# Kernel optimization log

Hardware: AMD Instinct MI355X
Metric: run time of the kernel (lower is better)

Reference implementation:

```python
import jax, jax.numpy as jnp
import numpy as np

N, TI, TO1 = 8, 200, 51
V, E, H, J, L = 1024, 512, 512, 512, 3
ENC_D = 512


def setup_inputs() -> dict:
    key = jax.random.key(0)
    ks = jax.random.split(key, 11)
    s = lambda k, shape, sc: jax.random.normal(k, shape, jnp.float32) * sc
    return {
        "enc_out": s(ks[0], (N, TI, ENC_D), 1.0),
        "tgt_pad": jax.random.randint(ks[1], (N, TO1), 0, V),
        "embed": s(ks[2], (V, E), 0.02),          # nn.Embedding weight
        "w_ih": s(ks[3], (L, 4 * H, E), 0.04),    # LSTM input-hidden (gate order i,f,g,o)
        "w_hh": s(ks[4], (L, 4 * H, H), 0.04),    # LSTM hidden-hidden
        "b_ih": s(ks[5], (L, 4 * H), 0.04),
        "b_hh": s(ks[6], (L, 4 * H), 0.04),
        "enc_w": s(ks[7], (J, ENC_D), 0.04),      # enc_proj (no bias)
        "dec_w": s(ks[8], (J, H), 0.04),          # dec_proj weight
        "dec_b": s(ks[9], (J,), 0.04),            # dec_proj bias
        "out_w": s(ks[10], (V, J), 0.04),         # output (no bias)
    }


def lstm_layer(x, wih, whh, bih, bhh):
    # x: [N, T, E] -> [N, T, H]; PyTorch LSTM gate order i, f, g, o
    n = x.shape[0]
    h0 = jnp.zeros((n, whh.shape[1]), x.dtype)
    c0 = jnp.zeros_like(h0)
    gin = jnp.einsum('nte,ge->ntg', x, wih) + bih + bhh  # precompute input contributions

    def step(carry, g_t):
        h, c = carry
        g = g_t + h @ whh.T
        i, f, gg, o = jnp.split(g, 4, axis=-1)
        c = jax.nn.sigmoid(f) * c + jax.nn.sigmoid(i) * jnp.tanh(gg)
        h = jax.nn.sigmoid(o) * jnp.tanh(c)
        return (h, c), h

    _, hs = jax.lax.scan(step, (h0, c0), jnp.swapaxes(gin, 0, 1))
    return jnp.swapaxes(hs, 0, 1)


def reference(enc_out, tgt_pad, embed, w_ih, w_hh, b_ih, b_hh, enc_w, dec_w, dec_b, out_w):
    # embedding lookup
    x = embed[tgt_pad]                                   # [N, To+1, E]
    # 3-layer unidirectional LSTM
    for l in range(w_ih.shape[0]):
        x = lstm_layer(x, w_ih[l], w_hh[l], b_ih[l], b_hh[l])
    # projections
    enc_p = jnp.einsum('ntd,jd->ntj', enc_out, enc_w)    # [N, Ti, J]
    dec_p = jnp.einsum('nud,jd->nuj', x, dec_w) + dec_b  # [N, To+1, J]
    # joint: broadcast add -> tanh -> output linear (no bias)
    add = enc_p[:, :, None, :] + dec_p[:, None, :, :]    # [N, Ti, To+1, J]
    return jnp.einsum('ntuj,vj->ntuv', jnp.tanh(add), out_w)  # [N, Ti, To+1, V]
```

## Files before the change

kernel.cpp:

```cpp
#include <hip/hip_runtime.h>
#include <cstdint>
#include <cstddef>

typedef __attribute__((ext_vector_type(4))) float f32x4;
typedef __attribute__((ext_vector_type(8))) short bf16x8;
typedef __attribute__((ext_vector_type(8))) unsigned short u16x8;
typedef __attribute__((ext_vector_type(4))) float float4v;
typedef __attribute__((ext_vector_type(2))) unsigned long long u64x2;
typedef unsigned long long ull;

#define NB   8
#define TIN  200
#define TO1  51
#define VSZ  1024
#define HSZ  512
static constexpr int MJOINT = NB * TIN * TO1;
static constexpr int MROWS  = TO1 * NB;

static constexpr size_t B_ENCBF = 0;
static constexpr size_t B_ENCW  = B_ENCBF + 1664ull*512*2;
static constexpr size_t B_DECW  = B_ENCW  + 512ull*512*2;
static constexpr size_t B_OUTW  = B_DECW  + 512ull*512*2;
static constexpr size_t B_WIH   = B_OUTW  + 1024ull*512*2;
static constexpr size_t B_WHH   = B_WIH   + 3ull*2048*512*2;
static constexpr size_t B_XTR   = B_WHH   + 3ull*2048*512*2;
static constexpr size_t B_BSUM  = B_XTR   + 4ull*408*512*2;
static constexpr size_t B_FLAGS = B_BSUM  + 3ull*2048*4;
static constexpr size_t B_ENCP  = B_FLAGS + 8192;
static constexpr size_t B_DECP  = B_ENCP  + 1664ull*512*4;
static constexpr size_t B_ABUF  = B_DECP  + 512ull*512*4;

__device__ __forceinline__ unsigned short f2bf(float f) {
  union { float f; unsigned u; } v; v.f = f;
  unsigned r = v.u + 0x7FFFu + ((v.u >> 16) & 1u);
  return (unsigned short)(r >> 16);
}
__device__ __forceinline__ float fast_tanh(float x) {
  float t = __expf(2.0f * x);
  return 1.0f - 2.0f / (t + 1.0f);
}
__device__ __forceinline__ float fast_sig(float x) {
  return 1.0f / (1.0f + __expf(-x));
}
__device__ __forceinline__ void gll16(const void* g, void* l) {
  __builtin_amdgcn_global_load_lds(
      (const __attribute__((address_space(1))) unsigned int*)g,
      (__attribute__((address_space(3))) unsigned int*)l, 16, 0, 0);
}
__device__ __forceinline__ void cvt8(const float* s, unsigned short* d) {
  const float4v* sp = (const float4v*)s;
  float4v x = sp[0], y = sp[1];
  u16x8 o;
  o[0]=f2bf(x[0]); o[1]=f2bf(x[1]); o[2]=f2bf(x[2]); o[3]=f2bf(x[3]);
  o[4]=f2bf(y[0]); o[5]=f2bf(y[1]); o[6]=f2bf(y[2]); o[7]=f2bf(y[3]);
  *(u16x8*)d = o;
}

static constexpr int N_ENC  = 102400;
static constexpr int N_ENCW = 32768;
static constexpr int N_DECW = 32768;
static constexpr int N_OUTW = 65536;
static constexpr int N_WIH  = 393216;
static constexpr int P0 = N_ENC, P1 = P0+N_ENCW, P2 = P1+N_DECW, P3 = P2+N_OUTW,
                     P4 = P3+N_WIH;

__global__ __launch_bounds__(256) void cvt_all(const float* __restrict__ enc,
                                               const float* __restrict__ encw,
                                               const float* __restrict__ decw,
                                               const float* __restrict__ outw,
                                               const float* __restrict__ wih,
                                               const float* __restrict__ whh,
                                               unsigned short* __restrict__ d_enc,
                                               unsigned short* __restrict__ d_encw,
                                               unsigned short* __restrict__ d_decw,
                                               unsigned short* __restrict__ d_outw,
                                               unsigned short* __restrict__ d_wih,
                                               unsigned short* __restrict__ d_whh,
                                               int* __restrict__ flags) {
  if (blockIdx.x == 0 && threadIdx.x < 96) flags[threadIdx.x * 16] = 0;
  int i = blockIdx.x * 256 + threadIdx.x;
  const float* s; unsigned short* d; int rel;
  if      (i < P0) { s = enc;  d = d_enc;  rel = i; }
  else if (i < P1) { s = encw; d = d_encw; rel = i - P0; }
  else if (i < P2) { s = decw; d = d_decw; rel = i - P1; }
  else if (i < P3) { s = outw; d = d_outw; rel = i - P2; }
  else if (i < P4) { s = wih;  d = d_wih;  rel = i - P3; }
  else             { s = whh;  d = d_whh;  rel = i - P4; }
  cvt8(s + (size_t)rel * 8, d + (size_t)rel * 8);
}

__global__ __launch_bounds__(256) void bsum_kernel(const float* __restrict__ a,
                                                   const float* __restrict__ b,
                                                   float* __restrict__ o, int n) {
  int i = blockIdx.x * 256 + threadIdx.x;
  if (i < n) o[i] = a[i] + b[i];
}

__global__ __launch_bounds__(256) void embed_kernel(const float* __restrict__ emb,
                                                    const int* __restrict__ tgt,
                                                    unsigned short* __restrict__ x0) {
  int idx = blockIdx.x * 256 + threadIdx.x;
  if (idx >= MROWS * 64) return;
  int m = idx >> 6, kc = (idx & 63) * 8;
  int t = m >> 3, n = m & 7;
  int v = tgt[n * TO1 + t];
  cvt8(emb + (size_t)v * 512 + kc, x0 + (size_t)m * 512 + kc);
}

__global__ __launch_bounds__(256) void gemm_bf16(const unsigned short* __restrict__ A,
                                                 const unsigned short* __restrict__ B,
                                                 float* __restrict__ C,
                                                 const float* __restrict__ bias,
                                                 int M, int N, int K) {
  __shared__ __align__(16) unsigned short lds[2][2][4096];
  const int tid = threadIdx.x;
  const int wave = tid >> 6, lane = tid & 63;
  const int lr = lane & 15, lg = lane >> 4;
  const int wm = (wave >> 1) * 64, wn = (wave & 1) * 64;
  const int xsl = (lg ^ (lr & 3)) << 3;

  const int nwg = gridDim.x * gridDim.y;
  const int id = blockIdx.y * gridDim.x + blockIdx.x;
  const int q = nwg >> 3, r = nwg & 7, xcd = id & 7, rest = id >> 3;
  const int nid = (xcd < r ? xcd * (q + 1) : r * (q + 1) + (xcd - r) * q) + rest;
  const size_t n0 = (size_t)(nid % gridDim.x) * 128;
  const size_t m0 = (size_t)(nid / gridDim.x) * 128;

  f32x4 acc[4][4];
#pragma unroll
  for (int i = 0; i < 4; ++i)
#pragma unroll
    for (int j = 0; j < 4; ++j) acc[i][j] = (f32x4){0.f, 0.f, 0.f, 0.f};

#define STAGE(bf, kt)                                                                 \
  do {                                                                                \
    _Pragma("unroll") for (int u = 0; u < 2; ++u) {                                   \
      const int s = u * 256 + tid;                                                    \
      const int row_ = s >> 2;                                                        \
      const int ch = (s & 3) ^ (row_ & 3);                                            \
      gll16(A + (m0 + row_) * (size_t)K + (kt) + ch * 8,                              \
            &lds[bf][0][(u * 256 + wave * 64) * 8]);                                  \
    }                                                                                 \
    _Pragma("unroll") for (int u = 0; u < 2; ++u) {                                   \
      const int s = u * 256 + tid;                                                    \
      const int row_ = s >> 2;                                                        \
      const int ch = (s & 3) ^ (row_ & 3);                                            \
      gll16(B + (n0 + row_) * (size_t)K + (kt) + ch * 8,                              \
            &lds[bf][1][(u * 256 + wave * 64) * 8]);                                  \
    }                                                                                 \
  } while (0)

  const int nt = K >> 5;
  int cur = 0;
  STAGE(0, 0);
  for (int t = 0; t < nt; ++t) {
    if (t + 1 < nt) {
      STAGE(cur ^ 1, (t + 1) * 32);
      asm volatile("s_waitcnt vmcnt(4)" ::: "memory");
    } else {
      asm volatile("s_waitcnt vmcnt(0)" ::: "memory");
    }
    __builtin_amdgcn_s_barrier();
    const unsigned short* As_ = lds[cur][0];
    const unsigned short* Bs_ = lds[cur][1];
    bf16x8 a[4], b[4];
#pragma unroll
    for (int i = 0; i < 4; ++i) a[i] = *(const bf16x8*)&As_[(wm + i * 16 + lr) * 32 + xsl];
#pragma unroll
    for (int j = 0; j < 4; ++j) b[j] = *(const bf16x8*)&Bs_[(wn + j * 16 + lr) * 32 + xsl];
    __builtin_amdgcn_s_setprio(1);
#pragma unroll
    for (int i = 0; i < 4; ++i)
#pragma unroll
      for (int j = 0; j < 4; ++j)
        acc[i][j] = __builtin_amdgcn_mfma_f32_16x16x32_bf16(a[i], b[j], acc[i][j], 0, 0, 0);
    __builtin_amdgcn_s_setprio(0);
    __builtin_amdgcn_s_barrier();
    cur ^= 1;
  }
#undef STAGE

  const int rq = lg * 4;
#pragma unroll
  for (int j = 0; j < 4; ++j) {
    const int col = (int)n0 + wn + j * 16 + lr;
    const float bv = bias ? bias[col] : 0.0f;
#pragma unroll
    for (int i = 0; i < 4; ++i) {
#pragma unroll
      for (int q2 = 0; q2 < 4; ++q2) {
        const long m = (long)m0 + wm + i * 16 + rq + q2;
        if (m < M) C[(size_t)m * N + col] = acc[i][j][q2] + bv;
      }
    }
  }
}

__global__ __launch_bounds__(512, 2) void gemm256(const unsigned short* __restrict__ A,
                                                  const unsigned short* __restrict__ B,
                                                  float* __restrict__ C,
                                                  int M, int N, int K) {
  __shared__ __align__(16) unsigned short lds[2][2][16384];
  const int tid = threadIdx.x;
  const int wave = tid >> 6, lane = tid & 63;
  const int lr = lane & 15, lg = lane >> 4;
  const int wr = (wave >> 2) * 128;
  const int wc = (wave & 3) * 64;

  const int nwg = gridDim.x * gridDim.y;
  const int id = blockIdx.y * gridDim.x + blockIdx.x;
  const int q = nwg >> 3, r = nwg & 7, xcd = id & 7, rest = id >> 3;
  const int nid = (xcd < r ? xcd * (q + 1) : r * (q + 1) + (xcd - r) * q) + rest;
  const size_t n0 = (size_t)(nid % gridDim.x) * 256;
  const size_t m0 = (size_t)(nid / gridDim.x) * 256;

  f32x4 acc[8][4];
#pragma unroll
  for (int i = 0; i < 8; ++i)
#pragma unroll
    for (int j = 0; j < 4; ++j) acc[i][j] = (f32x4){0.f, 0.f, 0.f, 0.f};

#define STG(bf, kt)                                                                    \
  do {                                                                                 \
    _Pragma("unroll") for (int u = 0; u < 4; ++u) {                                    \
      const int idx = u * 512 + tid;                                                   \
      const int row_ = idx >> 3;                                                       \
      const int ch = (idx & 7) ^ (row_ & 7);                                           \
      gll16(A + (m0 + row_) * (size_t)K + (kt) + ch * 8,                               \
            &lds[bf][0][(u * 512 + wave * 64) * 8]);                                   \
    }                                                                                  \
    _Pragma("unroll") for (int u = 0; u < 4; ++u) {                                    \
      const int idx = u * 512 + tid;                                                   \
      const int row_ = idx >> 3;                                                       \
      const int ch = (idx & 7) ^ (row_ & 7);                                           \
      gll16(B + (n0 + row_) * (size_t)K + (kt) + ch * 8,                               \
            &lds[bf][1][(u * 512 + wave * 64) * 8]);                                   \
    }                                                                                  \
  } while (0)

  const int nt = K >> 6;
  int cur = 0;
  STG(0, 0);
  for (int t = 0; t < nt; ++t) {
    if (t + 1 < nt) {
      STG(cur ^ 1, (t + 1) * 64);
      asm volatile("s_waitcnt vmcnt(8)" ::: "memory");
    } else {
      asm volatile("s_waitcnt vmcnt(0)" ::: "memory");
    }
    __builtin_amdgcn_s_barrier();
    const unsigned short* As_ = lds[cur][0];
    const unsigned short* Bs_ = lds[cur][1];
    bf16x8 b[4][2];
#pragma unroll
    for (int p = 0; p < 4; ++p) {
      if (p == 0) {
#pragma unroll
        for (int j = 0; j < 4; ++j) {
          const int rb = wc + j * 16 + lr;
          const int sw = rb & 7;
          b[j][0] = *(const bf16x8*)&Bs_[rb * 64 + ((lg ^ sw) << 3)];
          b[j][1] = *(const bf16x8*)&Bs_[rb * 64 + (((4 + lg) ^ sw) << 3)];
        }
      }
      bf16x8 a[2][2];
#pragma unroll
      for (int i2 = 0; i2 < 2; ++i2) {
        const int ra = wr + (p * 2 + i2) * 16 + lr;
        const int swa = ra & 7;
        a[i2][0] = *(const bf16x8*)&As_[ra * 64 + ((lg ^ swa) << 3)];
        a[i2][1] = *(const bf16x8*)&As_[ra * 64 + (((4 + lg) ^ swa) << 3)];
      }
      __builtin_amdgcn_s_setprio(1);
#pragma unroll
      for (int i2 = 0; i2 < 2; ++i2) {
        const int i = p * 2 + i2;
#pragma unroll
        for (int j = 0; j < 4; ++j) {
          acc[i][j] = __builtin_amdgcn_mfma_f32_16x16x32_bf16(a[i2][0], b[j][0], acc[i][j], 0, 0, 0);
          acc[i][j] = __builtin_amdgcn_mfma_f32_16x16x32_bf16(a[i2][1], b[j][1], acc[i][j], 0, 0, 0);
        }
      }
      __builtin_amdgcn_s_setprio(0);
      __builtin_amdgcn_s_barrier();
    }
    cur ^= 1;
  }
#undef STG

#pragma unroll
  for (int i = 0; i < 8; ++i) {
#pragma unroll
    for (int q2 = 0; q2 < 4; ++q2) {
      const long m = (long)m0 + wr + i * 16 + lg * 4 + q2;
      if (m < M) {
        float* crow = C + (size_t)m * N + n0 + wc;
#pragma unroll
        for (int j = 0; j < 4; ++j) crow[j * 16 + lr] = acc[i][j][q2];
      }
    }
  }
}

__global__ __launch_bounds__(256) void tanha_kernel(const float* __restrict__ encp,
                                                    const float* __restrict__ decp,
                                                    unsigned short* __restrict__ Ab) {
  size_t idx = (size_t)blockIdx.x * 256 + threadIdx.x;
  int m = (int)(idx >> 6);
  int kc = ((int)idx & 63) * 8;
  if (m >= 81664) return;
  u16x8 o;
  if (m >= MJOINT) {
    o[0]=0;o[1]=0;o[2]=0;o[3]=0;o[4]=0;o[5]=0;o[6]=0;o[7]=0;
  } else {
    int n = m / (TIN * TO1);
    int rem = m - n * (TIN * TO1);
    int t = rem / TO1;
    int u = rem - t * TO1;
    const float4v* ep = (const float4v*)(encp + ((size_t)n * TIN + t) * 512 + kc);
    const float4v* dp = (const float4v*)(decp + ((size_t)u * 8 + n) * 512 + kc);
    float4v e0 = ep[0], e1 = ep[1], d0 = dp[0], d1 = dp[1];
    o[0]=f2bf(fast_tanh(e0[0]+d0[0])); o[1]=f2bf(fast_tanh(e0[1]+d0[1]));
    o[2]=f2bf(fast_tanh(e0[2]+d0[2])); o[3]=f2bf(fast_tanh(e0[3]+d0[3]));
    o[4]=f2bf(fast_tanh(e1[0]+d1[0])); o[5]=f2bf(fast_tanh(e1[1]+d1[1]));
    o[6]=f2bf(fast_tanh(e1[2]+d1[2])); o[7]=f2bf(fast_tanh(e1[3]+d1[3]));
  }
  *(u16x8*)(Ab + (size_t)m * 512 + kc) = o;
}

__global__ __launch_bounds__(256) void rnn_enc_kernel(const unsigned short* __restrict__ wih,
                                                      const unsigned short* __restrict__ whh,
                                                      const float* __restrict__ bsum,
                                                      unsigned short* __restrict__ xtr,
                                                      int* __restrict__ flags,
                                                      const unsigned short* __restrict__ eA,
                                                      const unsigned short* __restrict__ eB,
                                                      float* __restrict__ eC) {
  __shared__ __align__(16) unsigned short w_s[64 * 1024];
  __shared__ __align__(16) unsigned short x_s[8 * 512];
  __shared__ __align__(16) unsigned short h_s[8 * 512];
  __shared__ float gates_s[4][8][16];

  const int tid = threadIdx.x;
  const int wave = tid >> 6, lane = tid & 63;
  const int lr = lane & 15, lg = lane >> 4;

  if (blockIdx.x >= 96) {
    unsigned short* eld = w_s;
    const int g = blockIdx.x - 96;
    const int wm = (wave >> 1) * 64, wn = (wave & 1) * 64;
    const int xsl = (lg ^ (lr & 3)) << 3;
    const int nwg = 52;
    const int q = nwg >> 3, r = nwg & 7, xcd = g & 7, rest = g >> 3;
    const int nid = (xcd < r ? xcd * (q + 1) : r * (q + 1) + (xcd - r) * q) + rest;
    const size_t n0 = (size_t)(nid & 3) * 128;
    const size_t m0 = (size_t)(nid >> 2) * 128;

    f32x4 acc[4][4];
#pragma unroll
    for (int i = 0; i < 4; ++i)
#pragma unroll
      for (int j = 0; j < 4; ++j) acc[i][j] = (f32x4){0.f, 0.f, 0.f, 0.f};

#define ESTG(bf, kt)                                                                   \
    do {                                                                               \
      _Pragma("unroll") for (int u = 0; u < 2; ++u) {                                  \
        const int s = u * 256 + tid;                                                   \
        const int row_ = s >> 2;                                                       \
        const int ch = (s & 3) ^ (row_ & 3);                                           \
        gll16(eA + (m0 + row_) * 512 + (kt) + ch * 8,                                  \
              &eld[(bf) * 8192 + (u * 256 + wave * 64) * 8]);                          \
      }                                                                                \
      _Pragma("unroll") for (int u = 0; u < 2; ++u) {                                  \
        const int s = u * 256 + tid;                                                   \
        const int row_ = s >> 2;                                                       \
        const int ch = (s & 3) ^ (row_ & 3);                                           \
        gll16(eB + (n0 + row_) * 512 + (kt) + ch * 8,                                  \
              &eld[(bf) * 8192 + 4096 + (u * 256 + wave * 64) * 8]);                   \
      }                                                                                \
    } while (0)

    int cur = 0;
    ESTG(0, 0);
    for (int t = 0; t < 16; ++t) {
      if (t + 1 < 16) {
        ESTG(cur ^ 1, (t + 1) * 32);
        asm volatile("s_waitcnt vmcnt(4)" ::: "memory");
      } else {
        asm volatile("s_waitcnt vmcnt(0)" ::: "memory");
      }
      __builtin_amdgcn_s_barrier();
      const unsigned short* As_ = eld + cur * 8192;
      const unsigned short* Bs_ = As_ + 4096;
      bf16x8 a[4], b[4];
#pragma unroll
      for (int i = 0; i < 4; ++i) a[i] = *(const bf16x8*)&As_[(wm + i * 16 + lr) * 32 + xsl];
#pragma unroll
      for (int j = 0; j < 4; ++j) b[j] = *(const bf16x8*)&Bs_[(wn + j * 16 + lr) * 32 + xsl];
      __builtin_amdgcn_s_setprio(1);
#pragma unroll
      for (int i = 0; i < 4; ++i)
#pragma unroll
        for (int j = 0; j < 4; ++j)
          acc[i][j] = __builtin_amdgcn_mfma_f32_16x16x32_bf16(a[i], b[j], acc[i][j], 0, 0, 0);
      __builtin_amdgcn_s_setprio(0);
      __builtin_amdgcn_s_barrier();
      cur ^= 1;
    }
#undef ESTG

    const int rq = lg * 4;
#pragma unroll
    for (int j = 0; j < 4; ++j) {
      const int col = (int)n0 + wn + j * 16 + lr;
#pragma unroll
      for (int i = 0; i < 4; ++i) {
#pragma unroll
        for (int q2 = 0; q2 < 4; ++q2) {
          const long m = (long)m0 + wm + i * 16 + rq + q2;
          eC[(size_t)m * 512 + col] = acc[i][j][q2];
        }
      }
    }
    return;
  }

  const int l = blockIdx.x >> 5;
  const int b32 = blockIdx.x & 31;
  const int hid0 = b32 << 4;
  const int r7 = lr & 7;
  const int rw = wave * 16 + lr;

  {
    const int rl = tid >> 2;
    const int qt = tid & 3;
    const size_t R = (size_t)l * 2048 + (size_t)(rl >> 4) * 512 + hid0 + (rl & 15);
    const unsigned short* s0 = wih + R * 512;
    const unsigned short* s1 = whh + R * 512;
#pragma unroll
    for (int i = 0; i < 32; ++i) {
      int c = qt * 32 + i;
      bf16x8 wv = (c < 64) ? *(const bf16x8*)&s0[c * 8] : *(const bf16x8*)&s1[(c - 64) * 8];
      *(bf16x8*)&w_s[rl * 1024 + ((c ^ (rl & 7)) << 3)] = wv;
    }
  }
  const float bias = bsum[(size_t)l * 2048 + (size_t)wave * 512 + hid0 + lr];

  const unsigned short* xin = xtr + (size_t)l * MROWS * 512;
  unsigned short* xout = xtr + (size_t)(l + 1) * MROWS * 512;
  float c_reg = 0.f;
  const int srow = tid >> 5;
  const int sc = tid & 31;
  __syncthreads();

#define ALOAD(P) __hip_atomic_load((P), __ATOMIC_RELAXED, __HIP_MEMORY_SCOPE_AGENT)

  f32x4 ax0, ax1;

  if (l > 0) {
    if (wave == 0) {
      for (;;) {
        bool ok_ = true;
        if (lane < 32)
          ok_ = ALOAD(&flags[((l - 1) * 32 + lane) * 16]) >= 1;
        if (__all(ok_)) break;
        __builtin_amdgcn_s_sleep(1);
      }
    }
  }
  __syncthreads();
  {
    const ull* px = (const ull*)(xin + (size_t)srow * 512);
#pragma unroll
    for (int k_ = 0; k_ < 2; ++k_) {
      const int c_ = sc + k_ * 32;
      ull v0 = ALOAD(px + c_ * 2), v1 = ALOAD(px + c_ * 2 + 1);
      *(u64x2*)&x_s[srow * 512 + ((c_ ^ srow) << 3)] = (u64x2){v0, v1};
    }
  }
  __syncthreads();
  ax0 = (f32x4){0.f, 0.f, 0.f, 0.f};
  ax1 = (f32x4){0.f, 0.f, 0.f, 0.f};
#pragma unroll
  for (int c16 = 0; c16 < 16; ++c16) {
    const int cc = c16 * 4 + lg;
    bf16x8 av = *(const bf16x8*)&x_s[r7 * 512 + ((cc ^ r7) << 3)];
    bf16x8 bv = *(const bf16x8*)&w_s[rw * 1024 + ((cc ^ r7) << 3)];
    if (c16 & 1) ax1 = __builtin_amdgcn_mfma_f32_16x16x32_bf16(av, bv, ax1, 0, 0, 0);
    else         ax0 = __builtin_amdgcn_mfma_f32_16x16x32_bf16(av, bv, ax0, 0, 0, 0);
  }

  for (int t = 0; t < TO1; ++t) {
    const bool doH = (t > 0);
    const bool doX = (t + 1 < TO1);
    if (doH || (doX && l > 0)) {
      if (wave == 0) {
        for (;;) {
          bool ok_ = true;
          if (lane < 32) {
            if (doH) ok_ = ALOAD(&flags[(l * 32 + lane) * 16]) >= t;
          } else {
            if (doX && l > 0)
              ok_ = ALOAD(&flags[((l - 1) * 32 + (lane - 32)) * 16]) >= t + 2;
          }
          if (__all(ok_)) break;
          __builtin_amdgcn_s_sleep(1);
        }
      }
    }
    __syncthreads();

    {
      ull vh[4], vx[4];
      const ull* ph = (const ull*)(xout + ((size_t)(t - 1) * 8 + srow) * 512);
      const ull* px = (const ull*)(xin + ((size_t)(t + 1) * 8 + srow) * 512);
#pragma unroll
      for (int k_ = 0; k_ < 2; ++k_) {
        const int c_ = sc + k_ * 32;
        if (doH) { vh[2 * k_] = ALOAD(ph + c_ * 2); vh[2 * k_ + 1] = ALOAD(ph + c_ * 2 + 1); }
        if (doX) { vx[2 * k_] = ALOAD(px + c_ * 2); vx[2 * k_ + 1] = ALOAD(px + c_ * 2 + 1); }
      }
#pragma unroll
      for (int k_ = 0; k_ < 2; ++k_) {
        const int c_ = sc + k_ * 32;
        if (doH) *(u64x2*)&h_s[srow * 512 + ((c_ ^ srow) << 3)] = (u64x2){vh[2 * k_], vh[2 * k_ + 1]};
        if (doX) *(u64x2*)&x_s[srow * 512 + ((c_ ^ srow) << 3)] = (u64x2){vx[2 * k_], vx[2 * k_ + 1]};
      }
    }
    __syncthreads();

    f32x4 acc0 = ax0, acc1 = ax1;
    if (doH) {
#pragma unroll
      for (int c16 = 0; c16 < 16; ++c16) {
        const int cc = c16 * 4 + lg;
        bf16x8 av = *(const bf16x8*)&h_s[r7 * 512 + ((cc ^ r7) << 3)];
        bf16x8 bv = *(const bf16x8*)&w_s[rw * 1024 + (((64 + cc) ^ r7) << 3)];
        if (c16 & 1) acc1 = __builtin_amdgcn_mfma_f32_16x16x32_bf16(av, bv, acc1, 0, 0, 0);
        else         acc0 = __builtin_amdgcn_mfma_f32_16x16x32_bf16(av, bv, acc0, 0, 0, 0);
      }
    }

    {
      f32x4 g = acc0 + acc1;
      const int nb4 = lg * 4;
#pragma unroll
      for (int q2 = 0; q2 < 4; ++q2) {
        int n = nb4 + q2;
        if (n < 8) gates_s[wave][n][lr] = g[q2] + bias;
      }
    }
    __syncthreads();
    if (tid < 128) {
      const int n = tid >> 4, j = tid & 15;
      float gi = gates_s[0][n][j], gf = gates_s[1][n][j];
      float gg = gates_s[2][n][j], go = gates_s[3][n][j];
      c_reg = fast_sig(gf) * c_reg + fast_sig(gi) * fast_tanh(gg);
      float ht = fast_sig(go) * fast_tanh(c_reg);
      float htn = __shfl_down(ht, 1);
      if (!(j & 1)) {
        unsigned pk = (unsigned)f2bf(ht) | ((unsigned)f2bf(htn) << 16);
        unsigned* dst = (unsigned*)(xout + ((size_t)t * 8 + n) * 512 + hid0 + j);
        __hip_atomic_store(dst, pk, __ATOMIC_RELAXED, __HIP_MEMORY_SCOPE_AGENT);
      }
    }
    asm volatile("s_waitcnt vmcnt(0)" ::: "memory");
    __syncthreads();
    if (tid == 0)
      __hip_atomic_store(&flags[(l * 32 + b32) * 16], t + 1,
                         __ATOMIC_RELAXED, __HIP_MEMORY_SCOPE_AGENT);

    if (doX) {
      ax0 = (f32x4){0.f, 0.f, 0.f, 0.f};
      ax1 = (f32x4){0.f, 0.f, 0.f, 0.f};
#pragma unroll
      for (int c16 = 0; c16 < 16; ++c16) {
        const int cc = c16 * 4 + lg;
        bf16x8 av = *(const bf16x8*)&x_s[r7 * 512 + ((cc ^ r7) << 3)];
        bf16x8 bv = *(const bf16x8*)&w_s[rw * 1024 + ((cc ^ r7) << 3)];
        if (c16 & 1) ax1 = __builtin_amdgcn_mfma_f32_16x16x32_bf16(av, bv, ax1, 0, 0, 0);
        else         ax0 = __builtin_amdgcn_mfma_f32_16x16x32_bf16(av, bv, ax0, 0, 0, 0);
      }
    }
  }
#undef ALOAD
}

extern "C" void kernel_launch(void* const* d_in, const int* in_sizes, int n_in,
                              void* d_out, int out_size, void* d_ws, size_t ws_size,
                              hipStream_t stream) {
  (void)in_sizes; (void)n_in; (void)out_size; (void)ws_size;
  const float* enc_out = (const float*)d_in[0];
  const int*   tgt     = (const int*)d_in[1];
  const float* embed   = (const float*)d_in[2];
  const float* w_ih    = (const float*)d_in[3];
  const float* w_hh    = (const float*)d_in[4];
  const float* b_ih    = (const float*)d_in[5];
  const float* b_hh    = (const float*)d_in[6];
  const float* enc_w   = (const float*)d_in[7];
  const float* dec_w   = (const float*)d_in[8];
  const float* dec_b   = (const float*)d_in[9];
  const float* out_w   = (const float*)d_in[10];

  char* ws = (char*)d_ws;
  unsigned short* enc_bf  = (unsigned short*)(ws + B_ENCBF);
  unsigned short* encw_bf = (unsigned short*)(ws + B_ENCW);
  unsigned short* decw_bf = (unsigned short*)(ws + B_DECW);
  unsigned short* outw_bf = (unsigned short*)(ws + B_OUTW);
  unsigned short* wih_bf  = (unsigned short*)(ws + B_WIH);
  unsigned short* whh_bf  = (unsigned short*)(ws + B_WHH);
  unsigned short* xtr     = (unsigned short*)(ws + B_XTR);
  float* bsum  = (float*)(ws + B_BSUM);
  int*   flags = (int*)(ws + B_FLAGS);
  float* encp  = (float*)(ws + B_ENCP);
  float* decp  = (float*)(ws + B_DECP);
  unsigned short* abuf = (unsigned short*)(ws + B_ABUF);
  float* Cout  = (float*)d_out;

  cvt_all<<<3984, 256, 0, stream>>>(enc_out, enc_w, dec_w, out_w, w_ih, w_hh,
                                    enc_bf, encw_bf, decw_bf, outw_bf, wih_bf, whh_bf,
                                    flags);
  bsum_kernel<<<24, 256, 0, stream>>>(b_ih, b_hh, bsum, 6144);
  embed_kernel<<<102, 256, 0, stream>>>(embed, tgt, xtr);

  rnn_enc_kernel<<<148, 256, 0, stream>>>(wih_bf, whh_bf, bsum, xtr, flags,
                                          enc_bf, encw_bf, encp);

  gemm_bf16<<<dim3(4, 4), 256, 0, stream>>>(xtr + 3ull * MROWS * 512, decw_bf, decp, dec_b,
                                            MROWS, 512, 512);
  tanha_kernel<<<20416, 256, 0, stream>>>(encp, decp, abuf);
  gemm256<<<dim3(4, 319), 512, 0, stream>>>(abuf, outw_bf, Cout, MJOINT, VSZ, 512);
}
```

Before: 345.0 us.

## Merge prep kernels into one launch and halve gemm256 K-tile to 32

Folds the bias-sum and embedding-gather kernels into the bf16 conversion kernel, using extra blocks, so three launches become one. Separately, the main output GEMM now stages 32-wide K slices instead of 64, which halves its LDS footprint and drops the inner per-phase barriers in favour of one barrier per K step. The smaller LDS use may allow more resident workgroups, but there are twice as many K iterations, each with a full barrier and less load-compute overlap per stage.

```diff
diff --git a/kernel.cpp b/kernel.cpp
--- a/kernel.cpp
+++ b/kernel.cpp
@@ -64,20 +64,41 @@
 static constexpr int P0 = N_ENC, P1 = P0+N_ENCW, P2 = P1+N_DECW, P3 = P2+N_OUTW,
                      P4 = P3+N_WIH;
 
-__global__ __launch_bounds__(256) void cvt_all(const float* __restrict__ enc,
-                                               const float* __restrict__ encw,
-                                               const float* __restrict__ decw,
-                                               const float* __restrict__ outw,
-                                               const float* __restrict__ wih,
-                                               const float* __restrict__ whh,
-                                               unsigned short* __restrict__ d_enc,
-                                               unsigned short* __restrict__ d_encw,
-                                               unsigned short* __restrict__ d_decw,
-                                               unsigned short* __restrict__ d_outw,
-                                               unsigned short* __restrict__ d_wih,
-                                               unsigned short* __restrict__ d_whh,
-                                               int* __restrict__ flags) {
+__global__ __launch_bounds__(256) void prep_all(const float* __restrict__ enc,
+                                                const float* __restrict__ encw,
+                                                const float* __restrict__ decw,
+                                                const float* __restrict__ outw,
+                                                const float* __restrict__ wih,
+                                                const float* __restrict__ whh,
+                                                const float* __restrict__ emb,
+                                                const int* __restrict__ tgt,
+                                                const float* __restrict__ bih,
+                                                const float* __restrict__ bhh,
+                                                unsigned short* __restrict__ d_enc,
+                                                unsigned short* __restrict__ d_encw,
+                                                unsigned short* __restrict__ d_decw,
+                                                unsigned short* __restrict__ d_outw,
+                                                unsigned short* __restrict__ d_wih,
+                                                unsigned short* __restrict__ d_whh,
+                                                unsigned short* __restrict__ x0,
+                                                float* __restrict__ bsum,
+                                                int* __restrict__ flags) {
   if (blockIdx.x == 0 && threadIdx.x < 96) flags[threadIdx.x * 16] = 0;
+  if (blockIdx.x >= 4086) {
+    int i = (blockIdx.x - 4086) * 2048 + threadIdx.x * 8;
+#pragma unroll
+    for (int k = 0; k < 8; ++k) bsum[i + k] = bih[i + k] + bhh[i + k];
+    return;
+  }
+  if (blockIdx.x >= 3984) {
+    int idx = (blockIdx.x - 3984) * 256 + threadIdx.x;
+    if (idx >= MROWS * 64) return;
+    int m = idx >> 6, kc = (idx & 63) * 8;
+    int t = m >> 3, n = m & 7;
+    int v = tgt[n * TO1 + t];
+    cvt8(emb + (size_t)v * 512 + kc, x0 + (size_t)m * 512 + kc);
+    return;
+  }
   int i = blockIdx.x * 256 + threadIdx.x;
   const float* s; unsigned short* d; int rel;
   if      (i < P0) { s = enc;  d = d_enc;  rel = i; }
@@ -87,24 +108,6 @@
   else if (i < P4) { s = wih;  d = d_wih;  rel = i - P3; }
   else             { s = whh;  d = d_whh;  rel = i - P4; }
   cvt8(s + (size_t)rel * 8, d + (size_t)rel * 8);
-}
-
-__global__ __launch_bounds__(256) void bsum_kernel(const float* __restrict__ a,
-                                                   const float* __restrict__ b,
-                                                   float* __restrict__ o, int n) {
-  int i = blockIdx.x * 256 + threadIdx.x;
-  if (i < n) o[i] = a[i] + b[i];
-}
-
-__global__ __launch_bounds__(256) void embed_kernel(const float* __restrict__ emb,
-                                                    const int* __restrict__ tgt,
-                                                    unsigned short* __restrict__ x0) {
-  int idx = blockIdx.x * 256 + threadIdx.x;
-  if (idx >= MROWS * 64) return;
-  int m = idx >> 6, kc = (idx & 63) * 8;
-  int t = m >> 3, n = m & 7;
-  int v = tgt[n * TO1 + t];
-  cvt8(emb + (size_t)v * 512 + kc, x0 + (size_t)m * 512 + kc);
 }
 
 __global__ __launch_bounds__(256) void gemm_bf16(const unsigned short* __restrict__ A,
@@ -200,7 +203,7 @@
                                                   const unsigned short* __restrict__ B,
                                                   float* __restrict__ C,
                                                   int M, int N, int K) {
-  __shared__ __align__(16) unsigned short lds[2][2][16384];
+  __shared__ __align__(16) unsigned short lds[2][2][8192];
   const int tid = threadIdx.x;
   const int wave = tid >> 6, lane = tid & 63;
   const int lr = lane & 15, lg = lane >> 4;
@@ -222,68 +225,52 @@
 
 #define STG(bf, kt)                                                                    \
   do {                                                                                 \
-    _Pragma("unroll") for (int u = 0; u < 4; ++u) {                                    \
+    _Pragma("unroll") for (int u = 0; u < 2; ++u) {                                    \
       const int idx = u * 512 + tid;                                                   \
-      const int row_ = idx >> 3;                                                       \
-      const int ch = (idx & 7) ^ (row_ & 7);                                           \
+      const int row_ = idx >> 2;                                                       \
+      const int ch = (idx & 3) ^ (row_ & 3);                                           \
       gll16(A + (m0 + row_) * (size_t)K + (kt) + ch * 8,                               \
             &lds[bf][0][(u * 512 + wave * 64) * 8]);                                   \
     }                                                                                  \
-    _Pragma("unroll") for (int u = 0; u < 4; ++u) {                                    \
+    _Pragma("unroll") for (int u = 0; u < 2; ++u) {                                    \
       const int idx = u * 512 + tid;                                                   \
-      const int row_ = idx >> 3;                                                       \
-      const int ch = (idx & 7) ^ (row_ & 7);                                           \
+      const int row_ = idx >> 2;                                                       \
+      const int ch = (idx & 3) ^ (row_ & 3);                                           \
       gll16(B + (n0 + row_) * (size_t)K + (kt) + ch * 8,                               \
             &lds[bf][1][(u * 512 + wave * 64) * 8]);                                   \
     }                                                                                  \
   } while (0)
 
-  const int nt = K >> 6;
+  const int nt = K >> 5;
   int cur = 0;
   STG(0, 0);
   for (int t = 0; t < nt; ++t) {
     if (t + 1 < nt) {
-      STG(cur ^ 1, (t + 1) * 64);
-      asm volatile("s_waitcnt vmcnt(8)" ::: "memory");
+      STG(cur ^ 1, (t + 1) * 32);
+      asm volatile("s_waitcnt vmcnt(4)" ::: "memory");
     } else {
       asm volatile("s_waitcnt vmcnt(0)" ::: "memory");
     }
     __builtin_amdgcn_s_barrier();
     const unsigned short* As_ = lds[cur][0];
     const unsigned short* Bs_ = lds[cur][1];
-    bf16x8 b[4][2];
-#pragma unroll
-    for (int p = 0; p < 4; ++p) {
-      if (p == 0) {
-#pragma unroll
-        for (int j = 0; j < 4; ++j) {
-          const int rb = wc + j * 16 + lr;
-          const int sw = rb & 7;
-          b[j][0] = *(const bf16x8*)&Bs_[rb * 64 + ((lg ^ sw) << 3)];
-          b[j][1] = *(const bf16x8*)&Bs_[rb * 64 + (((4 + lg) ^ sw) << 3)];
-        }
-      }
-      bf16x8 a[2][2];
-#pragma unroll
-      for (int i2 = 0; i2 < 2; ++i2) {
-        const int ra = wr + (p * 2 + i2) * 16 + lr;
-        const int swa = ra & 7;
-        a[i2][0] = *(const bf16x8*)&As_[ra * 64 + ((lg ^ swa) << 3)];
-        a[i2][1] = *(const bf16x8*)&As_[ra * 64 + (((4 + lg) ^ swa) << 3)];
-      }
-      __builtin_amdgcn_s_setprio(1);
-#pragma unroll
-      for (int i2 = 0; i2 < 2; ++i2) {
-        const int i = p * 2 + i2;
-#pragma unroll
-        for (int j = 0; j < 4; ++j) {
-          acc[i][j] = __builtin_amdgcn_mfma_f32_16x16x32_bf16(a[i2][0], b[j][0], acc[i][j], 0, 0, 0);
-          acc[i][j] = __builtin_amdgcn_mfma_f32_16x16x32_bf16(a[i2][1], b[j][1], acc[i][j], 0, 0, 0);
-        }
-      }
-      __builtin_amdgcn_s_setprio(0);
-      __builtin_amdgcn_s_barrier();
-    }
+    bf16x8 b[4];
+#pragma unroll
+    for (int j = 0; j < 4; ++j) {
+      const int rb = wc + j * 16 + lr;
+      b[j] = *(const bf16x8*)&Bs_[rb * 32 + ((lg ^ (rb & 3)) << 3)];
+    }
+    __builtin_amdgcn_s_setprio(1);
+#pragma unroll
+    for (int i = 0; i < 8; ++i) {
+      const int ra = wr + i * 16 + lr;
+      bf16x8 a0 = *(const bf16x8*)&As_[ra * 32 + ((lg ^ (ra & 3)) << 3)];
+#pragma unroll
+      for (int j = 0; j < 4; ++j)
+        acc[i][j] = __builtin_amdgcn_mfma_f32_16x16x32_bf16(a0, b[j], acc[i][j], 0, 0, 0);
+    }
+    __builtin_amdgcn_s_setprio(0);
+    __builtin_amdgcn_s_barrier();
     cur ^= 1;
   }
 #undef STG
@@ -617,11 +604,10 @@
   unsigned short* abuf = (unsigned short*)(ws + B_ABUF);
   float* Cout  = (float*)d_out;
 
-  cvt_all<<<3984, 256, 0, stream>>>(enc_out, enc_w, dec_w, out_w, w_ih, w_hh,
-                                    enc_bf, encw_bf, decw_bf, outw_bf, wih_bf, whh_bf,
-                                    flags);
-  bsum_kernel<<<24, 256, 0, stream>>>(b_ih, b_hh, bsum, 6144);
-  embed_kernel<<<102, 256, 0, stream>>>(embed, tgt, xtr);
+  prep_all<<<4089, 256, 0, stream>>>(enc_out, enc_w, dec_w, out_w, w_ih, w_hh,
+                                     embed, tgt, b_ih, b_hh,
+                                     enc_bf, encw_bf, decw_bf, outw_bf, wih_bf, whh_bf,
+                                     xtr, bsum, flags);
 
   rnn_enc_kernel<<<148, 256, 0, stream>>>(wih_bf, whh_bf, bsum, xtr, flags,
                                           enc_bf, encw_bf, encp);
```

Result: no change. 347.7 us (+0.8%).
